# Kernel optimization log

Measured on AMD Instinct MI355X. Metric: run time of the kernel, lower is better.

## Reference

```python
import jax, jax.numpy as jnp
import numpy as np

B = 4
N_PER_B = 65536
N = B * N_PER_B
GROUP_SIZE = 64
ORDER = 9  # min bits to cover grid size 512
C0, C1, C2 = 64, 128, 128


def hilbert_encode(coors, order):
    """Skilling AxesToTranspose, vectorized over N points, 3 dims -> int32 code."""
    n = 3
    X = [coors[:, i].astype(jnp.int32) for i in range(n)]
    M = 1 << (order - 1)
    Q = M
    while Q > 1:
        P = Q - 1
        for i in range(n):
            cond = (X[i] & Q) != 0
            if i == 0:
                X[0] = jnp.where(cond, X[0] ^ P, X[0])
            else:
                t = (X[0] ^ X[i]) & P
                x0 = jnp.where(cond, X[0] ^ P, X[0] ^ t)
                xi = jnp.where(cond, X[i], X[i] ^ t)
                X[0], X[i] = x0, xi
        Q >>= 1
    for i in range(1, n):
        X[i] = X[i] ^ X[i - 1]
    t = jnp.zeros_like(X[0])
    Q = M
    while Q > 1:
        t = jnp.where((X[n - 1] & Q) != 0, t ^ (Q - 1), t)
        Q >>= 1
    X = [x ^ t for x in X]
    # interleave transposed bits MSB-first: code has 3*order bits (27 < 31, fits int32)
    code = jnp.zeros_like(X[0])
    for b in range(order - 1, -1, -1):
        for i in range(n):
            code = (code << 1) | ((X[i] >> b) & 1)
    return code


def _mapping_indices(vox_coors):
    """Two Hilbert orderings (normal + reversed coord axes); per-batch stable grouping."""
    batch = vox_coors[:, 0]
    c1 = vox_coors[:, 1:4]
    c2 = vox_coors[:, 3:0:-1]  # [0,3,2,1] reverse of the xyz columns
    code1 = hilbert_encode(c1, ORDER)
    code2 = hilbert_encode(c2, ORDER)
    ind1 = jnp.lexsort((code1, batch))  # batch-major, curve-order minor
    ind2 = jnp.lexsort((code2, batch))
    inv1 = jnp.argsort(ind1)
    ind12 = inv1[ind2]  # maps ordering-1 arrangement to ordering-2 arrangement
    return ind1, ind12


def _block(p, x, params):
    """VoxFormer-style block: center pts per group, pos-encode, gate feats, local attn, FFN."""
    Wpos, bpos, Wq, Wk, Wv, Wo, Wout = params
    C = Wq.shape[0]
    gs = GROUP_SIZE
    pg = p.reshape(-1, gs, 3)
    e = (pg - pg.mean(axis=1, keepdims=True)).reshape(-1, 3) @ Wpos + bpos  # [N,C]
    h = (x * e).reshape(-1, gs, C)  # [G,gs,C]
    q, k, v = h @ Wq, h @ Wk, h @ Wv
    scores = jnp.einsum('gqc,gkc->gqk', q, k) / jnp.sqrt(jnp.asarray(C, q.dtype))
    attn = jax.nn.softmax(scores, axis=-1)
    o = jnp.einsum('gqk,gkc->gqc', attn, v).reshape(-1, C) @ Wo
    return jax.nn.relu(o) @ Wout  # [N,C_out]


def setup_inputs() -> dict:
    key = jax.random.key(0)
    ks = jax.random.split(key, 20)
    bcol = jnp.repeat(jnp.arange(B, dtype=jnp.int32), N_PER_B)
    z = jax.random.randint(ks[0], (N,), 0, 64, dtype=jnp.int32)
    y = jax.random.randint(ks[1], (N,), 0, 512, dtype=jnp.int32)
    x = jax.random.randint(ks[2], (N,), 0, 512, dtype=jnp.int32)
    vox_coors = jnp.stack([bcol, z, y, x], axis=1)
    vox_numbs = jnp.full((B,), N_PER_B, dtype=jnp.int32)
    vox_feats = jax.random.normal(ks[3], (N, C0), dtype=jnp.float32)
    pts_coors = jax.random.normal(ks[4], (N, 3), dtype=jnp.float32)
    s = lambda k, shape: jax.random.normal(k, shape, dtype=jnp.float32) / np.float32(np.sqrt(shape[0]))
    return dict(
        vox_numbs=vox_numbs, vox_coors=vox_coors, vox_feats=vox_feats, pts_coors=pts_coors,
        Wpos1=s(ks[5], (3, C0)), bpos1=jnp.zeros((C0,), jnp.float32),
        Wq1=s(ks[6], (C0, C0)), Wk1=s(ks[7], (C0, C0)), Wv1=s(ks[8], (C0, C0)),
        Wo1=s(ks[9], (C0, C0)), Wout1=s(ks[10], (C0, C1)),
        Wpos2=s(ks[11], (3, C1)), bpos2=jnp.zeros((C1,), jnp.float32),
        Wq2=s(ks[12], (C1, C1)), Wk2=s(ks[13], (C1, C1)), Wv2=s(ks[14], (C1, C1)),
        Wo2=s(ks[15], (C1, C1)), Wout2=s(ks[16], (C1, C2)),
    )


def reference(vox_numbs, vox_coors, vox_feats, pts_coors,
              Wpos1, bpos1, Wq1, Wk1, Wv1, Wo1, Wout1,
              Wpos2, bpos2, Wq2, Wk2, Wv2, Wo2, Wout2):
    ind1, ind12 = _mapping_indices(vox_coors)
    params = ((Wpos1, bpos1, Wq1, Wk1, Wv1, Wo1, Wout1),
              (Wpos2, bpos2, Wq2, Wk2, Wv2, Wo2, Wout2))
    for ind, prm in zip((ind1, ind12), params):
        vox_feats = vox_feats[ind]
        pts_coors = pts_coors[ind]
        vox_coors = vox_coors[ind]
        vox_feats = _block(pts_coors, vox_feats, prm)
    return vox_feats, pts_coors, vox_coors, vox_numbs
```

## Files before the change

### kernel.cpp

```cpp
#include <hip/hip_runtime.h>

using u64 = unsigned long long;
typedef _Float16 f16;
using f16x8 = __attribute__((ext_vector_type(8))) _Float16;
using f16x4 = __attribute__((ext_vector_type(4))) _Float16;
using f32x4 = __attribute__((ext_vector_type(4))) float;

__device__ __forceinline__ int hilbert3(int X0, int X1, int X2) {
  #pragma unroll
  for (int Q = 256; Q > 1; Q >>= 1) {
    const int P = Q - 1;
    if (X0 & Q) X0 ^= P;
    int t1 = (X0 ^ X1) & P;
    if (X1 & Q) X0 ^= P; else { X0 ^= t1; X1 ^= t1; }
    int t2 = (X0 ^ X2) & P;
    if (X2 & Q) X0 ^= P; else { X0 ^= t2; X2 ^= t2; }
  }
  X1 ^= X0;
  X2 ^= X1;
  int t = 0;
  #pragma unroll
  for (int Q = 256; Q > 1; Q >>= 1) if (X2 & Q) t ^= (Q - 1);
  X0 ^= t; X1 ^= t; X2 ^= t;
  int code = 0;
  #pragma unroll
  for (int b = 8; b >= 0; b--)
    code = (code << 3) | (((X0 >> b) & 1) << 2) | (((X1 >> b) & 1) << 1) | ((X2 >> b) & 1);
  return code;
}

__device__ __forceinline__ void cswap(u64& a, u64& b, bool up) {
  if ((a > b) == up) { u64 t = a; a = b; b = t; }
}

__global__ __launch_bounds__(1024) void sort_tile0(const int* __restrict__ vox,
                                                   u64* __restrict__ keys, int n,
                                                   int spanm1) {
  __shared__ u64 s[4096];
  const int base = blockIdx.x * 4096;
  const int bl = base & spanm1;
  #pragma unroll
  for (int m = 0; m < 4; m++) {
    const int e = base + threadIdx.x + m * 1024;
    const int isrc = e & (n - 1);
    const int4 c = ((const int4*)vox)[isrc];
    const unsigned code = (e < n) ? (unsigned)hilbert3(c.y, c.z, c.w)
                                  : (unsigned)hilbert3(c.w, c.z, c.y);
    s[threadIdx.x + m * 1024] =
        ((u64)(unsigned)c.x << 45) | ((u64)code << 18) | (unsigned)isrc;
  }
  __syncthreads();
  for (int k = 2; k <= 4096; k <<= 1) {
    for (int j = k >> 1; j >= 1; j >>= 1) {
      #pragma unroll
      for (int m = 0; m < 2; m++) {
        const int p = threadIdx.x + m * 1024;
        const int i = ((p & ~(j - 1)) << 1) | (p & (j - 1));
        const bool up = (((bl + i) & k) == 0);
        u64 a = s[i], b = s[i | j];
        if ((a > b) == up) { s[i] = b; s[i | j] = a; }
      }
      __syncthreads();
    }
  }
  #pragma unroll
  for (int m = 0; m < 4; m++)
    keys[base + threadIdx.x + m * 1024] = s[threadIdx.x + m * 1024];
}

template<int LEV>
__device__ __forceinline__ void gstepT(u64* __restrict__ keys, int t, int jlow,
                                       int k, int spanm1) {
  constexpr int S = 1 << LEV;
  const int i0 = ((t & ~(jlow - 1)) << LEV) | (t & (jlow - 1));
  const bool up = (((i0 & spanm1) & k) == 0);
  u64 x[S];
  #pragma unroll
  for (int m = 0; m < S; m++) x[m] = keys[i0 + (size_t)m * jlow];
  #pragma unroll
  for (int d = S >> 1; d >= 1; d >>= 1)
    #pragma unroll
    for (int m = 0; m < S; m++)
      if (!(m & d)) cswap(x[m], x[m | d], up);
  #pragma unroll
  for (int m = 0; m < S; m++) keys[i0 + (size_t)m * jlow] = x[m];
}

__global__ void bitonic_gN(u64* __restrict__ keys, int jlow, int lev, int k, int spanm1) {
  const int t = blockIdx.x * blockDim.x + threadIdx.x;
  switch (lev) {
    case 1: gstepT<1>(keys, t, jlow, k, spanm1); break;
    case 2: gstepT<2>(keys, t, jlow, k, spanm1); break;
    case 3: gstepT<3>(keys, t, jlow, k, spanm1); break;
    default: gstepT<4>(keys, t, jlow, k, spanm1); break;
  }
}

__global__ __launch_bounds__(1024) void merge_tile4(u64* __restrict__ keys, int k,
                                                    int spanm1) {
  __shared__ u64 s[4096];
  const int base = blockIdx.x * 4096;
  #pragma unroll
  for (int m = 0; m < 4; m++)
    s[threadIdx.x + m * 1024] = keys[base + threadIdx.x + m * 1024];
  __syncthreads();
  const bool up = (((base & spanm1) & k) == 0);
  for (int j = 2048; j >= 1; j >>= 1) {
    #pragma unroll
    for (int m = 0; m < 2; m++) {
      const int p = threadIdx.x + m * 1024;
      const int i = ((p & ~(j - 1)) << 1) | (p & (j - 1));
      u64 a = s[i], b = s[i | j];
      if ((a > b) == up) { s[i] = b; s[i | j] = a; }
    }
    __syncthreads();
  }
  #pragma unroll
  for (int m = 0; m < 4; m++)
    keys[base + threadIdx.x + m * 1024] = s[threadIdx.x + m * 1024];
}

__global__ void extract_inv_k(const u64* __restrict__ keys, const float* __restrict__ pts,
                              int* __restrict__ ind, int* __restrict__ inv,
                              float* __restrict__ pts1p, int n) {
  int t = blockIdx.x * blockDim.x + threadIdx.x;
  if (t >= n) return;
  int s = (int)(keys[t] & 0x3FFFFULL);
  ind[t] = s;
  inv[s] = t;
  pts1p[t * 3 + 0] = pts[s * 3 + 0];
  pts1p[t * 3 + 1] = pts[s * 3 + 1];
  pts1p[t * 3 + 2] = pts[s * 3 + 2];
}

__global__ void finish_k(const u64* __restrict__ keys2, const int* __restrict__ inv1,
                         int* __restrict__ g2, const float* __restrict__ pts,
                         const int* __restrict__ vox, const int* __restrict__ numbs,
                         float* __restrict__ out_pts, float* __restrict__ out_vox,
                         float* __restrict__ out_nb, int n, int B) {
  int t = blockIdx.x * blockDim.x + threadIdx.x;
  if (t >= n) return;
  int s = (int)(keys2[t] & 0x3FFFFULL);
  g2[t] = inv1[s];
  out_pts[t * 3 + 0] = pts[s * 3 + 0];
  out_pts[t * 3 + 1] = pts[s * 3 + 1];
  out_pts[t * 3 + 2] = pts[s * 3 + 2];
  const int4 v = ((const int4*)vox)[s];
  out_vox[t * 4 + 0] = (float)v.x;
  out_vox[t * 4 + 1] = (float)v.y;
  out_vox[t * 4 + 2] = (float)v.z;
  out_vox[t * 4 + 3] = (float)v.w;
  if (t < B) out_nb[t] = (float)numbs[t];
}

__global__ void prep_all(const float* __restrict__ Wq1, const float* __restrict__ Wk1,
                         const float* __restrict__ Wv1, const float* __restrict__ Wo1,
                         const float* __restrict__ Wout1,
                         const float* __restrict__ Wq2, const float* __restrict__ Wk2,
                         const float* __restrict__ Wv2, const float* __restrict__ Wo2,
                         const float* __restrict__ Wout2,
                         f16* __restrict__ A1a, f16* __restrict__ A2a, f16* __restrict__ A3a,
                         f16* __restrict__ A1b, f16* __restrict__ A2b, f16* __restrict__ A3b) {
  const int idx = blockIdx.x * blockDim.x + threadIdx.x;
  if (idx < 4096) {
    const int a = idx >> 6, b = idx & 63;
    float s1 = 0.f, s2 = 0.f;
    for (int c = 0; c < 64; c++) {
      s1 = fmaf(Wq1[b * 64 + c], Wk1[a * 64 + c], s1);
      s2 = fmaf(Wv1[b * 64 + c], Wo1[c * 64 + a], s2);
    }
    A1a[idx] = (f16)(s1 * 0.125f);
    A2a[idx] = (f16)s2;
  }
  if (idx < 8192) {
    const int o = idx >> 6, c = idx & 63;
    A3a[idx] = (f16)Wout1[c * 128 + o];
  }
  {
    const int a = idx >> 7, b = idx & 127;
    float s1 = 0.f, s2 = 0.f;
    for (int c = 0; c < 128; c++) {
      s1 = fmaf(Wq2[b * 128 + c], Wk2[a * 128 + c], s1);
      s2 = fmaf(Wv2[b * 128 + c], Wo2[c * 128 + a], s2);
    }
    A1b[idx] = (f16)(s1 * 0.08838834764831845f);
    A2b[idx] = (f16)s2;
    A3b[idx] = (f16)Wout2[b * 128 + a];
  }
}

__device__ __forceinline__ int swzb(int row) { return ((row ^ (row >> 3)) & 7) << 4; }

template<int M, int K, int AMODE>
__device__ __forceinline__ void gemmT(const f16* __restrict__ Ag, const f16* __restrict__ lA,
                                      const f16* __restrict__ lB, int w, int lane,
                                      f32x4 (&acc)[M / 64][4]) {
  constexpr int CT = M / 64;
  const int lr = lane & 15, lk = lane >> 4;
  #pragma unroll
  for (int ks = 0; ks < K / 32; ks++) {
    const int k0 = ks * 32 + lk * 8;
    f16x8 Af[CT];
    #pragma unroll
    for (int ct = 0; ct < CT; ct++) {
      const int c = lr + (w * CT + ct) * 16;
      if (AMODE == 0) {
        Af[ct] = *(const f16x8*)(Ag + (size_t)c * K + k0);
      } else if (AMODE == 1) {
        Af[ct] = *(const f16x8*)((const char*)lA + (((c * K + k0) * 2) ^ swzb(c)));
      } else {
        f16x8 a;
        #pragma unroll
        for (int e = 0; e < 8; e++) {
          const int j = k0 + e;
          a[e] = *(const f16*)((const char*)lA + (((j * M + c) * 2) ^ swzb(j)));
        }
        Af[ct] = a;
      }
    }
    f16x8 Bf[4];
    #pragma unroll
    for (int qt = 0; qt < 4; qt++) {
      const int q = lr + qt * 16;
      Bf[qt] = *(const f16x8*)((const char*)lB + (((q * K + k0) * 2) ^ swzb(q)));
    }
    #pragma unroll
    for (int ct = 0; ct < CT; ct++)
      #pragma unroll
      for (int qt = 0; qt < 4; qt++)
        acc[ct][qt] = __builtin_amdgcn_mfma_f32_16x16x32_f16(Af[ct], Bf[qt], acc[ct][qt], 0, 0, 0);
  }
}

template<int M, bool RELU>
__device__ __forceinline__ void storeT16(f16* __restrict__ dst, int w, int lane,
                                         const f32x4 (&acc)[M / 64][4]) {
  constexpr int CT = M / 64;
  #pragma unroll
  for (int ct = 0; ct < CT; ct++)
    #pragma unroll
    for (int qt = 0; qt < 4; qt++) {
      const int q = (lane & 15) + qt * 16;
      const int c0 = (w * CT + ct) * 16 + (lane >> 4) * 4;
      f16x4 v;
      #pragma unroll
      for (int r = 0; r < 4; r++) {
        float x = acc[ct][qt][r];
        if (RELU) x = fmaxf(x, 0.f);
        v[r] = (f16)x;
      }
      *(f16x4*)((char*)dst + (((q * M + c0) * 2) ^ swzb(q))) = v;
    }
}

template<int C, bool X16, bool OUT16>
__global__ __launch_bounds__(512, 4) void block_mfma(
    const int* __restrict__ idx_x, const float* __restrict__ ptsP,
    const void* __restrict__ xsrc,
    const float* __restrict__ Wpos, const float* __restrict__ bpos,
    const f16* __restrict__ A1, const f16* __restrict__ A2, const f16* __restrict__ A3,
    void* __restrict__ outp) {
  constexpr int CT = C / 64;
  constexpr int GSZ = 64 * C * 4 + 8192;
  extern __shared__ char smem_raw[];
  char* smem = smem_raw + (threadIdx.x >> 8) * GSZ;
  f16* bufH = (f16*)smem;
  f16* bufT = bufH + 64 * C;
  f16* scH  = bufT + 64 * C;

  const int g = blockIdx.x * 2 + (threadIdx.x >> 8);
  const int t = threadIdx.x & 255;
  const int lane = t & 63;
  const int w = t >> 6;
  const int lr = lane & 15, lk = lane >> 4;

  f16x8 A1f[C / 32][CT];
  #pragma unroll
  for (int ks = 0; ks < C / 32; ks++)
    #pragma unroll
    for (int ct = 0; ct < CT; ct++)
      A1f[ks][ct] = *(const f16x8*)(A1 + (size_t)(lr + (w * CT + ct) * 16) * C + ks * 32 + lk * 8);

  const int q = t >> 2, qq = t & 3;
  const int sx = idx_x[g * 64 + q];
  float xv[C / 4];
  if (X16) {
    #pragma unroll
    for (int i = 0; i < C / 32; i++) {
      f16x8 xr = *(const f16x8*)((const f16*)xsrc + (size_t)sx * C + qq * (C / 4) + i * 8);
      #pragma unroll
      for (int j = 0; j < 8; j++) xv[i * 8 + j] = (float)xr[j];
    }
  } else {
    #pragma unroll
    for (int i = 0; i < C / 16; i++) {
      float4 x0 = *(const float4*)((const float*)xsrc + (size_t)sx * C + qq * (C / 4) + i * 4);
      xv[i * 4 + 0] = x0.x; xv[i * 4 + 1] = x0.y; xv[i * 4 + 2] = x0.z; xv[i * 4 + 3] = x0.w;
    }
  }

  {
    float mx = ptsP[(g * 64 + lane) * 3 + 0];
    float my = ptsP[(g * 64 + lane) * 3 + 1];
    float mz = ptsP[(g * 64 + lane) * 3 + 2];
    #pragma unroll
    for (int o = 32; o > 0; o >>= 1) {
      mx += __shfl_xor(mx, o); my += __shfl_xor(my, o); mz += __shfl_xor(mz, o);
    }
    mx *= (1.f / 64.f); my *= (1.f / 64.f); mz *= (1.f / 64.f);

    const float d0 = ptsP[(g * 64 + q) * 3 + 0] - mx;
    const float d1 = ptsP[(g * 64 + q) * 3 + 1] - my;
    const float d2 = ptsP[(g * 64 + q) * 3 + 2] - mz;
    #pragma unroll
    for (int i = 0; i < C / 32; i++) {
      const int c0 = qq * (C / 4) + i * 8;
      f16x8 hv;
      #pragma unroll
      for (int jj = 0; jj < 8; jj += 4) {
        const float4 w0 = *(const float4*)(Wpos + 0 * C + c0 + jj);
        const float4 w1 = *(const float4*)(Wpos + 1 * C + c0 + jj);
        const float4 w2 = *(const float4*)(Wpos + 2 * C + c0 + jj);
        const float4 bb = *(const float4*)(bpos + c0 + jj);
        hv[jj + 0] = (f16)(xv[i * 8 + jj + 0] * fmaf(d0, w0.x, fmaf(d1, w1.x, fmaf(d2, w2.x, bb.x))));
        hv[jj + 1] = (f16)(xv[i * 8 + jj + 1] * fmaf(d0, w0.y, fmaf(d1, w1.y, fmaf(d2, w2.y, bb.y))));
        hv[jj + 2] = (f16)(xv[i * 8 + jj + 2] * fmaf(d0, w0.z, fmaf(d1, w1.z, fmaf(d2, w2.z, bb.z))));
        hv[jj + 3] = (f16)(xv[i * 8 + jj + 3] * fmaf(d0, w0.w, fmaf(d1, w1.w, fmaf(d2, w2.w, bb.w))));
      }
      *(f16x8*)((char*)bufH + (((q * C + c0) * 2) ^ swzb(q))) = hv;
    }
  }
  __syncthreads();

  {
    f32x4 acc[CT][4] = {};
    #pragma unroll
    for (int ks = 0; ks < C / 32; ks++) {
      const int k0 = ks * 32 + lk * 8;
      f16x8 Bf[4];
      #pragma unroll
      for (int qt = 0; qt < 4; qt++) {
        const int qr = lr + qt * 16;
        Bf[qt] = *(const f16x8*)((const char*)bufH + (((qr * C + k0) * 2) ^ swzb(qr)));
      }
      #pragma unroll
      for (int ct = 0; ct < CT; ct++)
        #pragma unroll
        for (int qt = 0; qt < 4; qt++)
          acc[ct][qt] = __builtin_amdgcn_mfma_f32_16x16x32_f16(A1f[ks][ct], Bf[qt], acc[ct][qt], 0, 0, 0);
    }
    storeT16<C, false>(bufT, w, lane, acc);
  }
  __syncthreads();

  {
    f32x4 acc[1][4] = {};
    gemmT<64, C, 1>(nullptr, bufH, bufT, w, lane, acc);
    #pragma unroll
    for (int qt = 0; qt < 4; qt++) {
      const int qr = lr + qt * 16;
      const int j0 = w * 16 + lk * 4;
      f16x4 v;
      #pragma unroll
      for (int r = 0; r < 4; r++) v[r] = (f16)acc[0][qt][r];
      *(f16x4*)((char*)scH + (((qr * 64 + j0) * 2) ^ swzb(qr))) = v;
    }
  }
  __syncthreads();

  {
    float v[16];
    float mxv = -3.0e38f;
    #pragma unroll
    for (int i = 0; i < 2; i++) {
      f16x8 x8 = *(const f16x8*)((const char*)scH + (((q * 64 + qq * 16 + i * 8) * 2) ^ swzb(q)));
      #pragma unroll
      for (int j = 0; j < 8; j++) {
        v[i * 8 + j] = (float)x8[j];
        mxv = fmaxf(mxv, v[i * 8 + j]);
      }
    }
    mxv = fmaxf(mxv, __shfl_xor(mxv, 1));
    mxv = fmaxf(mxv, __shfl_xor(mxv, 2));
    float s = 0.f;
    #pragma unroll
    for (int i = 0; i < 16; i++) { v[i] = __expf(v[i] - mxv); s += v[i]; }
    s += __shfl_xor(s, 1);
    s += __shfl_xor(s, 2);
    const float inv = 1.f / s;
    #pragma unroll
    for (int i = 0; i < 2; i++) {
      f16x8 pk;
      #pragma unroll
      for (int j = 0; j < 8; j++) pk[j] = (f16)(v[i * 8 + j] * inv);
      *(f16x8*)((char*)scH + (((q * 64 + qq * 16 + i * 8) * 2) ^ swzb(q))) = pk;
    }
  }
  __syncthreads();

  {
    f32x4 acc[CT][4] = {};
    gemmT<C, 64, 2>(nullptr, bufH, scH, w, lane, acc);
    storeT16<C, false>(bufT, w, lane, acc);
  }
  __syncthreads();

  {
    f32x4 acc[CT][4] = {};
    gemmT<C, C, 0>(A2, nullptr, bufT, w, lane, acc);
    storeT16<C, true>(bufH, w, lane, acc);
  }
  __syncthreads();

  {
    f32x4 acc[2][4] = {};
    gemmT<128, C, 0>(A3, nullptr, bufH, w, lane, acc);
    #pragma unroll
    for (int ct = 0; ct < 2; ct++)
      #pragma unroll
      for (int qt = 0; qt < 4; qt++) {
        const int qr = (lane & 15) + qt * 16;
        const int o0 = (w * 2 + ct) * 16 + (lane >> 4) * 4;
        const size_t row = (size_t)g * 64 + qr;
        if (OUT16) {
          f16x4 v;
          #pragma unroll
          for (int r = 0; r < 4; r++) v[r] = (f16)acc[ct][qt][r];
          *(f16x4*)((f16*)outp + row * 128 + o0) = v;
        } else {
          *(f32x4*)((float*)outp + row * 128 + o0) = acc[ct][qt];
        }
      }
  }
}

extern "C" void kernel_launch(void* const* d_in, const int* in_sizes, int n_in,
                              void* d_out, int out_size, void* d_ws, size_t ws_size,
                              hipStream_t stream) {
  const int*   vox_numbs = (const int*)d_in[0];
  const int*   vox_coors = (const int*)d_in[1];
  const float* vox_feats = (const float*)d_in[2];
  const float* pts_coors = (const float*)d_in[3];
  const float* Wpos1 = (const float*)d_in[4];
  const float* bpos1 = (const float*)d_in[5];
  const float* Wq1   = (const float*)d_in[6];
  const float* Wk1   = (const float*)d_in[7];
  const float* Wv1   = (const float*)d_in[8];
  const float* Wo1   = (const float*)d_in[9];
  const float* Wout1 = (const float*)d_in[10];
  const float* Wpos2 = (const float*)d_in[11];
  const float* bpos2 = (const float*)d_in[12];
  const float* Wq2   = (const float*)d_in[13];
  const float* Wk2   = (const float*)d_in[14];
  const float* Wv2   = (const float*)d_in[15];
  const float* Wo2   = (const float*)d_in[16];
  const float* Wout2 = (const float*)d_in[17];

  const int B = in_sizes[0];
  const int n = in_sizes[1] / 4;
  const int ngrp = n / 64;

  char* w = (char*)d_ws;
  auto alloc = [&](size_t bytes) {
    char* p = w;
    w += (bytes + 255) & ~(size_t)255;
    return p;
  };
  u64* keys    = (u64*)alloc((size_t)2 * n * 8);
  int* ind1    = (int*)alloc((size_t)n * 4);
  int* inv1    = (int*)alloc((size_t)n * 4);
  int* g2      = (int*)alloc((size_t)n * 4);
  float* pts1p = (float*)alloc((size_t)n * 3 * 4);
  f16* A1a     = (f16*)alloc(64 * 64 * 2);
  f16* A2a     = (f16*)alloc(64 * 64 * 2);
  f16* A3a     = (f16*)alloc(128 * 64 * 2);
  f16* A1b     = (f16*)alloc(128 * 128 * 2);
  f16* A2b     = (f16*)alloc(128 * 128 * 2);
  f16* A3b     = (f16*)alloc(128 * 128 * 2);
  f16* feats1  = (f16*)alloc((size_t)n * 128 * 2);
  u64* keys2   = keys + n;

  float* out_feats = (float*)d_out;
  float* out_pts   = out_feats + (size_t)n * 128;
  float* out_vox   = out_pts + (size_t)n * 3;
  float* out_nb    = out_vox + (size_t)n * 4;

  auto f64k  = block_mfma<64,  false, true>;
  auto f128k = block_mfma<128, true,  false>;
  hipFuncSetAttribute((const void*)f64k,  hipFuncAttributeMaxDynamicSharedMemorySize, 65536);
  hipFuncSetAttribute((const void*)f128k, hipFuncAttributeMaxDynamicSharedMemorySize, 98304);

  prep_all<<<64, 256, 0, stream>>>(Wq1, Wk1, Wv1, Wo1, Wout1, Wq2, Wk2, Wv2, Wo2, Wout2,
                                   A1a, A2a, A3a, A1b, A2b, A3b);

  int span = (B > 0) ? n / B : n;
  if (span < 8192 || (span & (span - 1)) != 0 || n % span != 0) span = n;
  const int spanm1 = span - 1;

  sort_tile0<<<2 * n / 4096, 1024, 0, stream>>>(vox_coors, keys, n, spanm1);
  for (int k = 8192; k <= span; k <<= 1) {
    int j = k >> 1;
    while (j >= 4096) {
      int lev = 1;
      while (lev < 4 && (j >> lev) >= 4096) lev++;
      const int jlow = j >> (lev - 1);
      const int nth = (2 * n) >> lev;
      bitonic_gN<<<nth / 256, 256, 0, stream>>>(keys, jlow, lev, k, spanm1);
      j = jlow >> 1;
    }
    merge_tile4<<<2 * n / 4096, 1024, 0, stream>>>(keys, k, spanm1);
  }

  extract_inv_k<<<(n + 255) / 256, 256, 0, stream>>>(keys, pts_coors, ind1, inv1, pts1p, n);
  finish_k<<<(n + 255) / 256, 256, 0, stream>>>(keys2, inv1, g2, pts_coors, vox_coors,
                                                vox_numbs, out_pts, out_vox, out_nb, n, B);

  block_mfma<64, false, true><<<ngrp / 2, 512, 2 * 24576, stream>>>(
      ind1, pts1p, vox_feats, Wpos1, bpos1, A1a, A2a, A3a, feats1);
  block_mfma<128, true, false><<<ngrp / 2, 512, 2 * 40960, stream>>>(
      g2, out_pts, feats1, Wpos2, bpos2, A1b, A2b, A3b, out_feats);
}
```

Measured before the change: 305.9 us.

## Preload weight fragments into registers, change LDS swizzle, add MFMA priority hints

Weight matrices A2 and A3 are now loaded into register fragments ahead of their GEMMs (A2 at kernel start, A3 before the barrier preceding its use) instead of being read from global memory inside the inner k-loop. The LDS XOR swizzle function is changed to a different bank-spreading pattern. s_setprio is raised around MFMA bursts, and the f16 input is kept packed rather than expanded to floats early. This aims to hide global-load latency and reduce LDS bank conflicts, at the cost of many more live VGPRs, which may cut occupancy under the 512-thread/4-block launch bound or cause spills.

```diff
diff --git a/kernel.cpp b/kernel.cpp
--- a/kernel.cpp
+++ b/kernel.cpp
@@ -189,10 +189,12 @@
   }
 }
 
-__device__ __forceinline__ int swzb(int row) { return ((row ^ (row >> 3)) & 7) << 4; }
+__device__ __forceinline__ int swzb(int row) {
+  return (((row & 7) ^ (((row >> 3) & 3) << 1)) << 4);
+}
 
 template<int M, int K, int AMODE>
-__device__ __forceinline__ void gemmT(const f16* __restrict__ Ag, const f16* __restrict__ lA,
+__device__ __forceinline__ void gemmT(const f16* __restrict__ lA,
                                       const f16* __restrict__ lB, int w, int lane,
                                       f32x4 (&acc)[M / 64][4]) {
   constexpr int CT = M / 64;
@@ -204,9 +206,7 @@
     #pragma unroll
     for (int ct = 0; ct < CT; ct++) {
       const int c = lr + (w * CT + ct) * 16;
-      if (AMODE == 0) {
-        Af[ct] = *(const f16x8*)(Ag + (size_t)c * K + k0);
-      } else if (AMODE == 1) {
+      if (AMODE == 1) {
         Af[ct] = *(const f16x8*)((const char*)lA + (((c * K + k0) * 2) ^ swzb(c)));
       } else {
         f16x8 a;
@@ -224,12 +224,51 @@
       const int q = lr + qt * 16;
       Bf[qt] = *(const f16x8*)((const char*)lB + (((q * K + k0) * 2) ^ swzb(q)));
     }
+    __builtin_amdgcn_s_setprio(1);
     #pragma unroll
     for (int ct = 0; ct < CT; ct++)
       #pragma unroll
       for (int qt = 0; qt < 4; qt++)
         acc[ct][qt] = __builtin_amdgcn_mfma_f32_16x16x32_f16(Af[ct], Bf[qt], acc[ct][qt], 0, 0, 0);
-  }
+    __builtin_amdgcn_s_setprio(0);
+  }
+}
+
+template<int M, int K>
+__device__ __forceinline__ void gemmPre(const f16x8 (&Af)[K / 32][M / 64],
+                                        const f16* __restrict__ lB, int lane,
+                                        f32x4 (&acc)[M / 64][4]) {
+  constexpr int CT = M / 64;
+  const int lr = lane & 15, lk = lane >> 4;
+  #pragma unroll
+  for (int ks = 0; ks < K / 32; ks++) {
+    const int k0 = ks * 32 + lk * 8;
+    f16x8 Bf[4];
+    #pragma unroll
+    for (int qt = 0; qt < 4; qt++) {
+      const int q = lr + qt * 16;
+      Bf[qt] = *(const f16x8*)((const char*)lB + (((q * K + k0) * 2) ^ swzb(q)));
+    }
+    __builtin_amdgcn_s_setprio(1);
+    #pragma unroll
+    for (int ct = 0; ct < CT; ct++)
+      #pragma unroll
+      for (int qt = 0; qt < 4; qt++)
+        acc[ct][qt] = __builtin_amdgcn_mfma_f32_16x16x32_f16(Af[ks][ct], Bf[qt], acc[ct][qt], 0, 0, 0);
+    __builtin_amdgcn_s_setprio(0);
+  }
+}
+
+template<int M, int K>
+__device__ __forceinline__ void loadA(const f16* __restrict__ Ag, int w, int lane,
+                                      f16x8 (&Af)[K / 32][M / 64]) {
+  constexpr int CT = M / 64;
+  const int lr = lane & 15, lk = lane >> 4;
+  #pragma unroll
+  for (int ks = 0; ks < K / 32; ks++)
+    #pragma unroll
+    for (int ct = 0; ct < CT; ct++)
+      Af[ks][ct] = *(const f16x8*)(Ag + (size_t)(lr + (w * CT + ct) * 16) * K + ks * 32 + lk * 8);
 }
 
 template<int M, bool RELU>
@@ -272,30 +311,25 @@
   const int t = threadIdx.x & 255;
   const int lane = t & 63;
   const int w = t >> 6;
-  const int lr = lane & 15, lk = lane >> 4;
-
-  f16x8 A1f[C / 32][CT];
-  #pragma unroll
-  for (int ks = 0; ks < C / 32; ks++)
-    #pragma unroll
-    for (int ct = 0; ct < CT; ct++)
-      A1f[ks][ct] = *(const f16x8*)(A1 + (size_t)(lr + (w * CT + ct) * 16) * C + ks * 32 + lk * 8);
+
+  f16x8 A1f[C / 32][CT], A2f[C / 32][CT];
+  loadA<C, C>(A1, w, lane, A1f);
+  loadA<C, C>(A2, w, lane, A2f);
 
   const int q = t >> 2, qq = t & 3;
   const int sx = idx_x[g * 64 + q];
-  float xv[C / 4];
+  f16x8 xr16[C / 32];
+  float xv32[X16 ? 1 : C / 4];
   if (X16) {
     #pragma unroll
-    for (int i = 0; i < C / 32; i++) {
-      f16x8 xr = *(const f16x8*)((const f16*)xsrc + (size_t)sx * C + qq * (C / 4) + i * 8);
-      #pragma unroll
-      for (int j = 0; j < 8; j++) xv[i * 8 + j] = (float)xr[j];
-    }
+    for (int i = 0; i < C / 32; i++)
+      xr16[i] = *(const f16x8*)((const f16*)xsrc + (size_t)sx * C + qq * (C / 4) + i * 8);
   } else {
     #pragma unroll
     for (int i = 0; i < C / 16; i++) {
       float4 x0 = *(const float4*)((const float*)xsrc + (size_t)sx * C + qq * (C / 4) + i * 4);
-      xv[i * 4 + 0] = x0.x; xv[i * 4 + 1] = x0.y; xv[i * 4 + 2] = x0.z; xv[i * 4 + 3] = x0.w;
+      xv32[i * 4 + 0] = x0.x; xv32[i * 4 + 1] = x0.y;
+      xv32[i * 4 + 2] = x0.z; xv32[i * 4 + 3] = x0.w;
     }
   }
 
@@ -322,10 +356,14 @@
         const float4 w1 = *(const float4*)(Wpos + 1 * C + c0 + jj);
         const float4 w2 = *(const float4*)(Wpos + 2 * C + c0 + jj);
         const float4 bb = *(const float4*)(bpos + c0 + jj);
-        hv[jj + 0] = (f16)(xv[i * 8 + jj + 0] * fmaf(d0, w0.x, fmaf(d1, w1.x, fmaf(d2, w2.x, bb.x))));
-        hv[jj + 1] = (f16)(xv[i * 8 + jj + 1] * fmaf(d0, w0.y, fmaf(d1, w1.y, fmaf(d2, w2.y, bb.y))));
-        hv[jj + 2] = (f16)(xv[i * 8 + jj + 2] * fmaf(d0, w0.z, fmaf(d1, w1.z, fmaf(d2, w2.z, bb.z))));
-        hv[jj + 3] = (f16)(xv[i * 8 + jj + 3] * fmaf(d0, w0.w, fmaf(d1, w1.w, fmaf(d2, w2.w, bb.w))));
+        float xa = X16 ? (float)xr16[i][jj + 0] : xv32[i * 8 + jj + 0];
+        float xb = X16 ? (float)xr16[i][jj + 1] : xv32[i * 8 + jj + 1];
+        float xc = X16 ? (float)xr16[i][jj + 2] : xv32[i * 8 + jj + 2];
+        float xd = X16 ? (float)xr16[i][jj + 3] : xv32[i * 8 + jj + 3];
+        hv[jj + 0] = (f16)(xa * fmaf(d0, w0.x, fmaf(d1, w1.x, fmaf(d2, w2.x, bb.x))));
+        hv[jj + 1] = (f16)(xb * fmaf(d0, w0.y, fmaf(d1, w1.y, fmaf(d2, w2.y, bb.y))));
+        hv[jj + 2] = (f16)(xc * fmaf(d0, w0.z, fmaf(d1, w1.z, fmaf(d2, w2.z, bb.z))));
+        hv[jj + 3] = (f16)(xd * fmaf(d0, w0.w, fmaf(d1, w1.w, fmaf(d2, w2.w, bb.w))));
       }
       *(f16x8*)((char*)bufH + (((q * C + c0) * 2) ^ swzb(q))) = hv;
     }
@@ -334,28 +372,15 @@
 
   {
     f32x4 acc[CT][4] = {};
-    #pragma unroll
-    for (int ks = 0; ks < C / 32; ks++) {
-      const int k0 = ks * 32 + lk * 8;
-      f16x8 Bf[4];
-      #pragma unroll
-      for (int qt = 0; qt < 4; qt++) {
-        const int qr = lr + qt * 16;
-        Bf[qt] = *(const f16x8*)((const char*)bufH + (((qr * C + k0) * 2) ^ swzb(qr)));
-      }
-      #pragma unroll
-      for (int ct = 0; ct < CT; ct++)
-        #pragma unroll
-        for (int qt = 0; qt < 4; qt++)
-          acc[ct][qt] = __builtin_amdgcn_mfma_f32_16x16x32_f16(A1f[ks][ct], Bf[qt], acc[ct][qt], 0, 0, 0);
-    }
+    gemmPre<C, C>(A1f, bufH, lane, acc);
     storeT16<C, false>(bufT, w, lane, acc);
   }
   __syncthreads();
 
   {
     f32x4 acc[1][4] = {};
-    gemmT<64, C, 1>(nullptr, bufH, bufT, w, lane, acc);
+    gemmT<64, C, 1>(bufH, bufT, w, lane, acc);
+    const int lr = lane & 15, lk = lane >> 4;
     #pragma unroll
     for (int qt = 0; qt < 4; qt++) {
       const int qr = lr + qt * 16;
@@ -400,21 +425,24 @@
 
   {
     f32x4 acc[CT][4] = {};
-    gemmT<C, 64, 2>(nullptr, bufH, scH, w, lane, acc);
+    gemmT<C, 64, 2>(bufH, scH, w, lane, acc);
     storeT16<C, false>(bufT, w, lane, acc);
   }
+
+  f16x8 A3f[C / 32][2];
+  loadA<128, C>(A3, w, lane, A3f);
   __syncthreads();
 
   {
     f32x4 acc[CT][4] = {};
-    gemmT<C, C, 0>(A2, nullptr, bufT, w, lane, acc);
+    gemmPre<C, C>(A2f, bufT, lane, acc);
     storeT16<C, true>(bufH, w, lane, acc);
   }
   __syncthreads();
 
   {
     f32x4 acc[2][4] = {};
-    gemmT<128, C, 0>(A3, nullptr, bufH, w, lane, acc);
+    gemmPre<128, C>(A3f, bufH, lane, acc);
     #pragma unroll
     for (int ct = 0; ct < 2; ct++)
       #pragma unroll
```

Measured after the change: 322.8 us. 1.06x slower.

## Restructure attention block so each wave owns 16 query rows end-to-end

Applied to the files above, without the earlier changes.

The per-group block kernel is rewritten so each of four waves processes its own 16 query rows through the whole chain (projection, scores, softmax, PV, Wo, Wout). Intermediates go through a small per-wave LDS scratch instead of block-wide buffers, which removes most __syncthreads. Softmax now runs in registers on the MFMA accumulators with cross-lane shuffles. A transposed copy of H is written to LDS for the PV product, and weights are read from global/L1 per MFMA rather than preloaded. Launches move from two groups per 512-thread block to one group per 256-thread block with less shared memory. The costs are redundant weight loads per wave, scalar f16 LDS transposed writes, and scalar global output stores.

```diff
diff --git a/kernel.cpp b/kernel.cpp
--- a/kernel.cpp
+++ b/kernel.cpp
@@ -189,117 +189,65 @@
   }
 }
 
-__device__ __forceinline__ int swzb(int row) { return ((row ^ (row >> 3)) & 7) << 4; }
-
-template<int M, int K, int AMODE>
-__device__ __forceinline__ void gemmT(const f16* __restrict__ Ag, const f16* __restrict__ lA,
-                                      const f16* __restrict__ lB, int w, int lane,
-                                      f32x4 (&acc)[M / 64][4]) {
-  constexpr int CT = M / 64;
-  const int lr = lane & 15, lk = lane >> 4;
-  #pragma unroll
-  for (int ks = 0; ks < K / 32; ks++) {
-    const int k0 = ks * 32 + lk * 8;
-    f16x8 Af[CT];
-    #pragma unroll
-    for (int ct = 0; ct < CT; ct++) {
-      const int c = lr + (w * CT + ct) * 16;
-      if (AMODE == 0) {
-        Af[ct] = *(const f16x8*)(Ag + (size_t)c * K + k0);
-      } else if (AMODE == 1) {
-        Af[ct] = *(const f16x8*)((const char*)lA + (((c * K + k0) * 2) ^ swzb(c)));
-      } else {
-        f16x8 a;
-        #pragma unroll
-        for (int e = 0; e < 8; e++) {
-          const int j = k0 + e;
-          a[e] = *(const f16*)((const char*)lA + (((j * M + c) * 2) ^ swzb(j)));
-        }
-        Af[ct] = a;
-      }
-    }
-    f16x8 Bf[4];
-    #pragma unroll
-    for (int qt = 0; qt < 4; qt++) {
-      const int q = lr + qt * 16;
-      Bf[qt] = *(const f16x8*)((const char*)lB + (((q * K + k0) * 2) ^ swzb(q)));
-    }
-    #pragma unroll
-    for (int ct = 0; ct < CT; ct++)
-      #pragma unroll
-      for (int qt = 0; qt < 4; qt++)
-        acc[ct][qt] = __builtin_amdgcn_mfma_f32_16x16x32_f16(Af[ct], Bf[qt], acc[ct][qt], 0, 0, 0);
-  }
-}
-
-template<int M, bool RELU>
-__device__ __forceinline__ void storeT16(f16* __restrict__ dst, int w, int lane,
-                                         const f32x4 (&acc)[M / 64][4]) {
-  constexpr int CT = M / 64;
-  #pragma unroll
-  for (int ct = 0; ct < CT; ct++)
-    #pragma unroll
-    for (int qt = 0; qt < 4; qt++) {
-      const int q = (lane & 15) + qt * 16;
-      const int c0 = (w * CT + ct) * 16 + (lane >> 4) * 4;
-      f16x4 v;
-      #pragma unroll
-      for (int r = 0; r < 4; r++) {
-        float x = acc[ct][qt][r];
-        if (RELU) x = fmaxf(x, 0.f);
-        v[r] = (f16)x;
-      }
-      *(f16x4*)((char*)dst + (((q * M + c0) * 2) ^ swzb(q))) = v;
-    }
-}
-
-template<int C, bool X16, bool OUT16>
-__global__ __launch_bounds__(512, 4) void block_mfma(
+__device__ __forceinline__ int swzb(int row) {
+  return (((row & 7) ^ (((row >> 3) & 3) << 1)) << 4);
+}
+
+template<int ROWLEN>
+__device__ __forceinline__ f16x8 ldRow(const f16* b, int row, int k0) {
+  return *(const f16x8*)((const char*)b + (((row * ROWLEN + k0) * 2) ^ swzb(row)));
+}
+
+template<int ROWLEN, bool RELU>
+__device__ __forceinline__ void rtWrite(f16* s, int lr, int lk, int c0, f32x4 v) {
+  #pragma unroll
+  for (int r = 0; r < 4; r++) {
+    const int row = lk * 4 + r;
+    float x = v[r];
+    if (RELU) x = fmaxf(x, 0.f);
+    *(f16*)((char*)s + (((row * ROWLEN + c0 + lr) * 2) ^ swzb(row))) = (f16)x;
+  }
+}
+
+template<int C, bool X16, bool OUT16, int MINW>
+__global__ __launch_bounds__(256, MINW) void block_mfma(
     const int* __restrict__ idx_x, const float* __restrict__ ptsP,
     const void* __restrict__ xsrc,
     const float* __restrict__ Wpos, const float* __restrict__ bpos,
     const f16* __restrict__ A1, const f16* __restrict__ A2, const f16* __restrict__ A3,
     void* __restrict__ outp) {
-  constexpr int CT = C / 64;
-  constexpr int GSZ = 64 * C * 4 + 8192;
-  extern __shared__ char smem_raw[];
-  char* smem = smem_raw + (threadIdx.x >> 8) * GSZ;
-  f16* bufH = (f16*)smem;
-  f16* bufT = bufH + 64 * C;
-  f16* scH  = bufT + 64 * C;
-
-  const int g = blockIdx.x * 2 + (threadIdx.x >> 8);
-  const int t = threadIdx.x & 255;
+  constexpr int KT = C / 32;
+  constexpr int CTL = C / 16;
+  extern __shared__ char smem[];
+  f16* bufH  = (f16*)smem;
+  f16* bufHT = bufH + 64 * C;
+  f16* scr   = bufHT + 64 * C;
+
+  const int g = blockIdx.x;
+  const int t = threadIdx.x;
   const int lane = t & 63;
   const int w = t >> 6;
   const int lr = lane & 15, lk = lane >> 4;
-
-  f16x8 A1f[C / 32][CT];
-  #pragma unroll
-  for (int ks = 0; ks < C / 32; ks++)
-    #pragma unroll
-    for (int ct = 0; ct < CT; ct++)
-      A1f[ks][ct] = *(const f16x8*)(A1 + (size_t)(lr + (w * CT + ct) * 16) * C + ks * 32 + lk * 8);
-
   const int q = t >> 2, qq = t & 3;
-  const int sx = idx_x[g * 64 + q];
-  float xv[C / 4];
-  if (X16) {
-    #pragma unroll
-    for (int i = 0; i < C / 32; i++) {
-      f16x8 xr = *(const f16x8*)((const f16*)xsrc + (size_t)sx * C + qq * (C / 4) + i * 8);
-      #pragma unroll
-      for (int j = 0; j < 8; j++) xv[i * 8 + j] = (float)xr[j];
-    }
-  } else {
-    #pragma unroll
-    for (int i = 0; i < C / 16; i++) {
-      float4 x0 = *(const float4*)((const float*)xsrc + (size_t)sx * C + qq * (C / 4) + i * 4);
-      xv[i * 4 + 0] = x0.x; xv[i * 4 + 1] = x0.y; xv[i * 4 + 2] = x0.z; xv[i * 4 + 3] = x0.w;
-    }
-  }
-
-  {
+  f16* myS = scr + w * 16 * C;
+
+  {
+    const int sx = idx_x[g * 64 + q];
+    float xv[C / 4];
+    if (X16) {
+      #pragma unroll
+      for (int i = 0; i < C / 32; i++) {
+        f16x8 xr = *(const f16x8*)((const f16*)xsrc + (size_t)sx * C + qq * (C / 4) + i * 8);
+        #pragma unroll
+        for (int j = 0; j < 8; j++) xv[i * 8 + j] = (float)xr[j];
+      }
+    } else {
+      #pragma unroll
+      for (int i = 0; i < C / 16; i++) {
+        float4 x0 = *(const float4*)((const float*)xsrc + (size_t)sx * C + qq * (C / 4) + i * 4);
+        xv[i * 4 + 0] = x0.x; xv[i * 4 + 1] = x0.y; xv[i * 4 + 2] = x0.z; xv[i * 4 + 3] = x0.w;
+      }
+    }
     float mx = ptsP[(g * 64 + lane) * 3 + 0];
     float my = ptsP[(g * 64 + lane) * 3 + 1];
     float mz = ptsP[(g * 64 + lane) * 3 + 2];
@@ -308,7 +256,6 @@
       mx += __shfl_xor(mx, o); my += __shfl_xor(my, o); mz += __shfl_xor(mz, o);
     }
     mx *= (1.f / 64.f); my *= (1.f / 64.f); mz *= (1.f / 64.f);
-
     const float d0 = ptsP[(g * 64 + q) * 3 + 0] - mx;
     const float d1 = ptsP[(g * 64 + q) * 3 + 1] - my;
     const float d2 = ptsP[(g * 64 + q) * 3 + 2] - mz;
@@ -328,108 +275,136 @@
         hv[jj + 3] = (f16)(xv[i * 8 + jj + 3] * fmaf(d0, w0.w, fmaf(d1, w1.w, fmaf(d2, w2.w, bb.w))));
       }
       *(f16x8*)((char*)bufH + (((q * C + c0) * 2) ^ swzb(q))) = hv;
+      #pragma unroll
+      for (int jj = 0; jj < 8; jj++)
+        *(f16*)((char*)bufHT + ((((c0 + jj) * 64 + q) * 2) ^ swzb(c0 + jj))) = hv[jj];
     }
   }
   __syncthreads();
 
-  {
-    f32x4 acc[CT][4] = {};
-    #pragma unroll
-    for (int ks = 0; ks < C / 32; ks++) {
-      const int k0 = ks * 32 + lk * 8;
-      f16x8 Bf[4];
-      #pragma unroll
-      for (int qt = 0; qt < 4; qt++) {
-        const int qr = lr + qt * 16;
-        Bf[qt] = *(const f16x8*)((const char*)bufH + (((qr * C + k0) * 2) ^ swzb(qr)));
-      }
-      #pragma unroll
-      for (int ct = 0; ct < CT; ct++)
-        #pragma unroll
-        for (int qt = 0; qt < 4; qt++)
-          acc[ct][qt] = __builtin_amdgcn_mfma_f32_16x16x32_f16(A1f[ks][ct], Bf[qt], acc[ct][qt], 0, 0, 0);
-    }
-    storeT16<C, false>(bufT, w, lane, acc);
-  }
-  __syncthreads();
-
-  {
-    f32x4 acc[1][4] = {};
-    gemmT<64, C, 1>(nullptr, bufH, bufT, w, lane, acc);
-    #pragma unroll
-    for (int qt = 0; qt < 4; qt++) {
-      const int qr = lr + qt * 16;
-      const int j0 = w * 16 + lk * 4;
-      f16x4 v;
-      #pragma unroll
-      for (int r = 0; r < 4; r++) v[r] = (f16)acc[0][qt][r];
-      *(f16x4*)((char*)scH + (((qr * 64 + j0) * 2) ^ swzb(qr))) = v;
-    }
-  }
-  __syncthreads();
-
-  {
-    float v[16];
+  const int qoff = w * 16;
+
+  f16x8 hA[KT];
+  #pragma unroll
+  for (int kt = 0; kt < KT; kt++) hA[kt] = ldRow<C>(bufH, qoff + lr, kt * 32 + lk * 8);
+  {
+    f32x4 acc[CTL];
+    #pragma unroll
+    for (int ct = 0; ct < CTL; ct++) acc[ct] = (f32x4){0.f, 0.f, 0.f, 0.f};
+    #pragma unroll
+    for (int ct = 0; ct < CTL; ct++)
+      #pragma unroll
+      for (int kt = 0; kt < KT; kt++) {
+        const f16x8 Bw = *(const f16x8*)(A1 + (size_t)(ct * 16 + lr) * C + kt * 32 + lk * 8);
+        acc[ct] = __builtin_amdgcn_mfma_f32_16x16x32_f16(hA[kt], Bw, acc[ct], 0, 0, 0);
+      }
+    #pragma unroll
+    for (int ct = 0; ct < CTL; ct++) rtWrite<C, false>(myS, lr, lk, ct * 16, acc[ct]);
+  }
+  f16x8 t1f[KT];
+  #pragma unroll
+  for (int kt = 0; kt < KT; kt++) t1f[kt] = ldRow<C>(myS, lr, kt * 32 + lk * 8);
+
+  f32x4 accS[4];
+  #pragma unroll
+  for (int jt = 0; jt < 4; jt++) accS[jt] = (f32x4){0.f, 0.f, 0.f, 0.f};
+  #pragma unroll
+  for (int jt = 0; jt < 4; jt++)
+    #pragma unroll
+    for (int kt = 0; kt < KT; kt++) {
+      const f16x8 Bh = ldRow<C>(bufH, jt * 16 + lr, kt * 32 + lk * 8);
+      accS[jt] = __builtin_amdgcn_mfma_f32_16x16x32_f16(t1f[kt], Bh, accS[jt], 0, 0, 0);
+    }
+
+  {
     float mxv = -3.0e38f;
     #pragma unroll
-    for (int i = 0; i < 2; i++) {
-      f16x8 x8 = *(const f16x8*)((const char*)scH + (((q * 64 + qq * 16 + i * 8) * 2) ^ swzb(q)));
-      #pragma unroll
-      for (int j = 0; j < 8; j++) {
-        v[i * 8 + j] = (float)x8[j];
-        mxv = fmaxf(mxv, v[i * 8 + j]);
-      }
-    }
+    for (int jt = 0; jt < 4; jt++)
+      #pragma unroll
+      for (int r = 0; r < 4; r++) mxv = fmaxf(mxv, accS[jt][r]);
     mxv = fmaxf(mxv, __shfl_xor(mxv, 1));
     mxv = fmaxf(mxv, __shfl_xor(mxv, 2));
+    mxv = fmaxf(mxv, __shfl_xor(mxv, 4));
+    mxv = fmaxf(mxv, __shfl_xor(mxv, 8));
     float s = 0.f;
     #pragma unroll
-    for (int i = 0; i < 16; i++) { v[i] = __expf(v[i] - mxv); s += v[i]; }
+    for (int jt = 0; jt < 4; jt++)
+      #pragma unroll
+      for (int r = 0; r < 4; r++) {
+        accS[jt][r] = __expf(accS[jt][r] - mxv);
+        s += accS[jt][r];
+      }
     s += __shfl_xor(s, 1);
     s += __shfl_xor(s, 2);
+    s += __shfl_xor(s, 4);
+    s += __shfl_xor(s, 8);
     const float inv = 1.f / s;
     #pragma unroll
-    for (int i = 0; i < 2; i++) {
-      f16x8 pk;
-      #pragma unroll
-      for (int j = 0; j < 8; j++) pk[j] = (f16)(v[i * 8 + j] * inv);
-      *(f16x8*)((char*)scH + (((q * 64 + qq * 16 + i * 8) * 2) ^ swzb(q))) = pk;
-    }
-  }
-  __syncthreads();
-
-  {
-    f32x4 acc[CT][4] = {};
-    gemmT<C, 64, 2>(nullptr, bufH, scH, w, lane, acc);
-    storeT16<C, false>(bufT, w, lane, acc);
-  }
-  __syncthreads();
-
-  {
-    f32x4 acc[CT][4] = {};
-    gemmT<C, C, 0>(A2, nullptr, bufT, w, lane, acc);
-    storeT16<C, true>(bufH, w, lane, acc);
-  }
-  __syncthreads();
-
-  {
-    f32x4 acc[2][4] = {};
-    gemmT<128, C, 0>(A3, nullptr, bufH, w, lane, acc);
-    #pragma unroll
-    for (int ct = 0; ct < 2; ct++)
-      #pragma unroll
-      for (int qt = 0; qt < 4; qt++) {
-        const int qr = (lane & 15) + qt * 16;
-        const int o0 = (w * 2 + ct) * 16 + (lane >> 4) * 4;
-        const size_t row = (size_t)g * 64 + qr;
-        if (OUT16) {
-          f16x4 v;
-          #pragma unroll
-          for (int r = 0; r < 4; r++) v[r] = (f16)acc[ct][qt][r];
-          *(f16x4*)((f16*)outp + row * 128 + o0) = v;
-        } else {
-          *(f32x4*)((float*)outp + row * 128 + o0) = acc[ct][qt];
-        }
+    for (int jt = 0; jt < 4; jt++) {
+      f32x4 v = accS[jt];
+      v[0] *= inv; v[1] *= inv; v[2] *= inv; v[3] *= inv;
+      rtWrite<64, false>(myS, lr, lk, jt * 16, v);
+    }
+  }
+  f16x8 paf[2];
+  #pragma unroll
+  for (int jt2 = 0; jt2 < 2; jt2++) paf[jt2] = ldRow<64>(myS, lr, jt2 * 32 + lk * 8);
+
+  {
+    f32x4 acc[CTL];
+    #pragma unroll
+    for (int ct = 0; ct < CTL; ct++) acc[ct] = (f32x4){0.f, 0.f, 0.f, 0.f};
+    #pragma unroll
+    for (int ct = 0; ct < CTL; ct++)
+      #pragma unroll
+      for (int jt2 = 0; jt2 < 2; jt2++) {
+        const f16x8 Bt = ldRow<64>(bufHT, ct * 16 + lr, jt2 * 32 + lk * 8);
+        acc[ct] = __builtin_amdgcn_mfma_f32_16x16x32_f16(paf[jt2], Bt, acc[ct], 0, 0, 0);
+      }
+    #pragma unroll
+    for (int ct = 0; ct < CTL; ct++) rtWrite<C, false>(myS, lr, lk, ct * 16, acc[ct]);
+  }
+  f16x8 t2f[KT];
+  #pragma unroll
+  for (int kt = 0; kt < KT; kt++) t2f[kt] = ldRow<C>(myS, lr, kt * 32 + lk * 8);
+
+  {
+    f32x4 acc[CTL];
+    #pragma unroll
+    for (int ct = 0; ct < CTL; ct++) acc[ct] = (f32x4){0.f, 0.f, 0.f, 0.f};
+    #pragma unroll
+    for (int ct = 0; ct < CTL; ct++)
+      #pragma unroll
+      for (int kt = 0; kt < KT; kt++) {
+        const f16x8 Bw = *(const f16x8*)(A2 + (size_t)(ct * 16 + lr) * C + kt * 32 + lk * 8);
+        acc[ct] = __builtin_amdgcn_mfma_f32_16x16x32_f16(t2f[kt], Bw, acc[ct], 0, 0, 0);
+      }
+    #pragma unroll
+    for (int ct = 0; ct < CTL; ct++) rtWrite<C, true>(myS, lr, lk, ct * 16, acc[ct]);
+  }
+  f16x8 of[KT];
+  #pragma unroll
+  for (int kt = 0; kt < KT; kt++) of[kt] = ldRow<C>(myS, lr, kt * 32 + lk * 8);
+
+  {
+    f32x4 acc[8];
+    #pragma unroll
+    for (int ot = 0; ot < 8; ot++) acc[ot] = (f32x4){0.f, 0.f, 0.f, 0.f};
+    #pragma unroll
+    for (int ot = 0; ot < 8; ot++)
+      #pragma unroll
+      for (int kt = 0; kt < KT; kt++) {
+        const f16x8 Bw = *(const f16x8*)(A3 + (size_t)(ot * 16 + lr) * C + kt * 32 + lk * 8);
+        acc[ot] = __builtin_amdgcn_mfma_f32_16x16x32_f16(of[kt], Bw, acc[ot], 0, 0, 0);
+      }
+    #pragma unroll
+    for (int ot = 0; ot < 8; ot++)
+      #pragma unroll
+      for (int r = 0; r < 4; r++) {
+        const size_t row = (size_t)g * 64 + qoff + lk * 4 + r;
+        const int col = ot * 16 + lr;
+        if (OUT16) ((f16*)outp)[row * 128 + col] = (f16)acc[ot][r];
+        else       ((float*)outp)[row * 128 + col] = acc[ot][r];
       }
   }
 }
@@ -485,10 +460,10 @@
   float* out_vox   = out_pts + (size_t)n * 3;
   float* out_nb    = out_vox + (size_t)n * 4;
 
-  auto f64k  = block_mfma<64,  false, true>;
-  auto f128k = block_mfma<128, true,  false>;
-  hipFuncSetAttribute((const void*)f64k,  hipFuncAttributeMaxDynamicSharedMemorySize, 65536);
-  hipFuncSetAttribute((const void*)f128k, hipFuncAttributeMaxDynamicSharedMemorySize, 98304);
+  auto f64k  = block_mfma<64,  false, true,  4>;
+  auto f128k = block_mfma<128, true,  false, 3>;
+  hipFuncSetAttribute((const void*)f64k,  hipFuncAttributeMaxDynamicSharedMemorySize, 32768);
+  hipFuncSetAttribute((const void*)f128k, hipFuncAttributeMaxDynamicSharedMemorySize, 65536);
 
   prep_all<<<64, 256, 0, stream>>>(Wq1, Wk1, Wv1, Wo1, Wout1, Wq2, Wk2, Wv2, Wo2, Wout2,
                                    A1a, A2a, A3a, A1b, A2b, A3b);
@@ -515,8 +490,8 @@
   finish_k<<<(n + 255) / 256, 256, 0, stream>>>(keys2, inv1, g2, pts_coors, vox_coors,
                                                 vox_numbs, out_pts, out_vox, out_nb, n, B);
 
-  block_mfma<64, false, true><<<ngrp / 2, 512, 2 * 24576, stream>>>(
+  block_mfma<64, false, true, 4><<<ngrp, 256, 3 * 64 * 64 * 2, stream>>>(
       ind1, pts1p, vox_feats, Wpos1, bpos1, A1a, A2a, A3a, feats1);
-  block_mfma<128, true, false><<<ngrp / 2, 512, 2 * 40960, stream>>>(
+  block_mfma<128, true, false, 3><<<ngrp, 256, 3 * 64 * 128 * 2, stream>>>(
       g2, out_pts, feats1, Wpos2, bpos2, A1b, A2b, A3b, out_feats);
 }
```

Result: slower. 474.0 us (+54.9%).

## Use one group per 256-thread block, new LDS swizzle, hoist global A-fragment loads

Applied to the files above, without the earlier changes.

Block kernels now launch one 64-point group per 256-thread workgroup instead of packing two groups into a 512-thread workgroup, halving per-block LDS so more workgroups can be resident. The LDS swizzle function is changed to a different XOR pattern to alter bank-conflict behavior. For the global-A GEMM mode, all A fragments are loaded up front before the MFMA loop, trading registers for fewer load stalls interleaved with compute.

```diff
diff --git a/kernel.cpp b/kernel.cpp
--- a/kernel.cpp
+++ b/kernel.cpp
@@ -189,24 +189,49 @@
   }
 }
 
-__device__ __forceinline__ int swzb(int row) { return ((row ^ (row >> 3)) & 7) << 4; }
+__device__ __forceinline__ int swzb(int row) {
+  return (((row & 7) ^ (((row >> 3) & 3) << 1)) << 4);
+}
 
 template<int M, int K, int AMODE>
 __device__ __forceinline__ void gemmT(const f16* __restrict__ Ag, const f16* __restrict__ lA,
                                       const f16* __restrict__ lB, int w, int lane,
                                       f32x4 (&acc)[M / 64][4]) {
   constexpr int CT = M / 64;
+  constexpr int KT = K / 32;
   const int lr = lane & 15, lk = lane >> 4;
-  #pragma unroll
-  for (int ks = 0; ks < K / 32; ks++) {
+  if (AMODE == 0) {
+    f16x8 Af[KT][CT];
+    #pragma unroll
+    for (int ks = 0; ks < KT; ks++)
+      #pragma unroll
+      for (int ct = 0; ct < CT; ct++)
+        Af[ks][ct] = *(const f16x8*)(Ag + (size_t)(lr + (w * CT + ct) * 16) * K + ks * 32 + lk * 8);
+    #pragma unroll
+    for (int ks = 0; ks < KT; ks++) {
+      const int k0 = ks * 32 + lk * 8;
+      f16x8 Bf[4];
+      #pragma unroll
+      for (int qt = 0; qt < 4; qt++) {
+        const int q = lr + qt * 16;
+        Bf[qt] = *(const f16x8*)((const char*)lB + (((q * K + k0) * 2) ^ swzb(q)));
+      }
+      #pragma unroll
+      for (int ct = 0; ct < CT; ct++)
+        #pragma unroll
+        for (int qt = 0; qt < 4; qt++)
+          acc[ct][qt] = __builtin_amdgcn_mfma_f32_16x16x32_f16(Af[ks][ct], Bf[qt], acc[ct][qt], 0, 0, 0);
+    }
+    return;
+  }
+  #pragma unroll
+  for (int ks = 0; ks < KT; ks++) {
     const int k0 = ks * 32 + lk * 8;
     f16x8 Af[CT];
     #pragma unroll
     for (int ct = 0; ct < CT; ct++) {
       const int c = lr + (w * CT + ct) * 16;
-      if (AMODE == 0) {
-        Af[ct] = *(const f16x8*)(Ag + (size_t)c * K + k0);
-      } else if (AMODE == 1) {
+      if (AMODE == 1) {
         Af[ct] = *(const f16x8*)((const char*)lA + (((c * K + k0) * 2) ^ swzb(c)));
       } else {
         f16x8 a;
@@ -254,22 +279,20 @@
 }
 
 template<int C, bool X16, bool OUT16>
-__global__ __launch_bounds__(512, 4) void block_mfma(
+__global__ __launch_bounds__(256, 4) void block_mfma(
     const int* __restrict__ idx_x, const float* __restrict__ ptsP,
     const void* __restrict__ xsrc,
     const float* __restrict__ Wpos, const float* __restrict__ bpos,
     const f16* __restrict__ A1, const f16* __restrict__ A2, const f16* __restrict__ A3,
     void* __restrict__ outp) {
   constexpr int CT = C / 64;
-  constexpr int GSZ = 64 * C * 4 + 8192;
-  extern __shared__ char smem_raw[];
-  char* smem = smem_raw + (threadIdx.x >> 8) * GSZ;
+  extern __shared__ char smem[];
   f16* bufH = (f16*)smem;
   f16* bufT = bufH + 64 * C;
   f16* scH  = bufT + 64 * C;
 
-  const int g = blockIdx.x * 2 + (threadIdx.x >> 8);
-  const int t = threadIdx.x & 255;
+  const int g = blockIdx.x;
+  const int t = threadIdx.x;
   const int lane = t & 63;
   const int w = t >> 6;
   const int lr = lane & 15, lk = lane >> 4;
@@ -488,7 +511,7 @@
   auto f64k  = block_mfma<64,  false, true>;
   auto f128k = block_mfma<128, true,  false>;
   hipFuncSetAttribute((const void*)f64k,  hipFuncAttributeMaxDynamicSharedMemorySize, 65536);
-  hipFuncSetAttribute((const void*)f128k, hipFuncAttributeMaxDynamicSharedMemorySize, 98304);
+  hipFuncSetAttribute((const void*)f128k, hipFuncAttributeMaxDynamicSharedMemorySize, 65536);
 
   prep_all<<<64, 256, 0, stream>>>(Wq1, Wk1, Wv1, Wo1, Wout1, Wq2, Wk2, Wv2, Wo2, Wout2,
                                    A1a, A2a, A3a, A1b, A2b, A3b);
@@ -515,8 +538,8 @@
   finish_k<<<(n + 255) / 256, 256, 0, stream>>>(keys2, inv1, g2, pts_coors, vox_coors,
                                                 vox_numbs, out_pts, out_vox, out_nb, n, B);
 
-  block_mfma<64, false, true><<<ngrp / 2, 512, 2 * 24576, stream>>>(
+  block_mfma<64, false, true><<<ngrp, 256, 24576, stream>>>(
       ind1, pts1p, vox_feats, Wpos1, bpos1, A1a, A2a, A3a, feats1);
-  block_mfma<128, true, false><<<ngrp / 2, 512, 2 * 40960, stream>>>(
+  block_mfma<128, true, false><<<ngrp, 256, 40960, stream>>>(
       g2, out_pts, feats1, Wpos2, bpos2, A1b, A2b, A3b, out_feats);
 }
```

New measurement: 299.5 us. 1.02x faster.
